# Kernel tuning notes

Hardware: AMD Instinct MI355X
Metric: run time of the kernel (lower is better)

The kernel has to match this reference:

```python
import jax, jax.numpy as jnp
import numpy as np

B, N, D_IN, D_MODEL = 8, 384, 512, 512


def gen_masking_matrix(n):
    # Vectorized port of the numba _gen_matrix: a[i, j, k] True iff k lies in the
    # 'geometric attention' reachability band between query i and key j.
    I = np.arange(n)[:, None, None]
    J = np.arange(n)[None, :, None]
    K = np.arange(n)[None, None, :]
    lt = (I < J) & (((K > I) & (K < J)) | ((K >= 2 * I - J + 1) & (K < I)))
    gt = (I > J) & (((K > J) & (K < I)) | ((K > I) & (K <= 2 * I - J)))
    return jnp.asarray(lt | gt)  # (n, n, n) bool


def setup_inputs() -> dict:
    key = jax.random.key(0)
    ks = jax.random.split(key, 8)
    s_in = 1.0 / np.sqrt(D_IN)
    return {
        "h": jax.random.normal(ks[0], (B, N, D_IN), jnp.float32),
        "mask": jnp.ones((B, N), jnp.float32),
        "Wq": jax.random.normal(ks[1], (D_MODEL, D_IN), jnp.float32) * s_in,
        "bq": jax.random.normal(ks[2], (D_MODEL,), jnp.float32) * 0.01,
        "Wk": jax.random.normal(ks[3], (D_MODEL, D_IN), jnp.float32) * s_in,
        "wlr": jax.random.normal(ks[4], (1, D_IN), jnp.float32) * s_in,
        "blr": jnp.zeros((1,), jnp.float32),
        "wrl": jax.random.normal(ks[5], (1, D_IN), jnp.float32) * s_in,
        "brl": jnp.zeros((1,), jnp.float32),
        "alpha": jnp.array([1.0 / np.sqrt(D_MODEL)], jnp.float32),
        "beta": jnp.array([1.0], jnp.float32),
        "gamma": jnp.array([0.0], jnp.float32),
        "masking_matrix": gen_masking_matrix(N),
    }


def reference(h, mask, Wq, bq, Wk, wlr, blr, wrl, brl, alpha, beta, gamma, masking_matrix):
    n = h.shape[1]
    dt = h.dtype
    q = h @ Wq.T + bq                       # (B, n, d_model)
    k = h @ Wk.T                            # (B, n, d_model)
    left = h @ wlr.T + blr                  # (B, n, 1)
    right = h @ wrl.T + brl                 # (B, n, 1)
    iu = jnp.triu(jnp.ones((n, n), dt))
    il = jnp.tril(jnp.ones((n, n), dt), -1)
    d = left * iu + right * il              # (B, n, n)
    scores = jnp.einsum("bnd,bmd->bnm", q, k)
    raw = jnp.clip(alpha * scores + beta * d + gamma, -16.0, 14.0)
    log_p = jax.nn.log_sigmoid(raw)         # log sigmoid(raw)
    log_1mp = jnp.log1p(-jnp.exp(log_p))    # log(1 - sigmoid(raw))
    # a[b,i,j] = sum_k mask[i,j,k] * log_1mp[b,i,k] + log_p[b,i,j]
    a = jnp.einsum("ijk,bik->bij", masking_matrix.astype(dt), log_1mp) + log_p
    r = a - 10000.0 * jnp.eye(n, dtype=dt)
    alignment_mask = mask[:, None, :] * mask[:, :, None]
    return r, alignment_mask
```

## Files before the change

kernel.cpp:

```cpp
#include <hip/hip_runtime.h>
#include <math.h>

#define N_SEQ 384
#define DIM 512
#define BATCH 8
#define M_ROWS (BATCH * N_SEQ)
#define QK_COLS (2 * DIM)

typedef short v8s __attribute__((ext_vector_type(8)));
typedef float v4f __attribute__((ext_vector_type(4)));

__device__ inline unsigned short f2bf(float f) {
    union { float f; unsigned u; } c; c.f = f;
    unsigned u = c.u;
    u += 0x7fffu + ((u >> 16) & 1u);
    return (unsigned short)(u >> 16);
}

__global__ __launch_bounds__(256) void prep(
    const float* __restrict__ h, const float* __restrict__ Wq,
    const float* __restrict__ Wk, const float* __restrict__ wlr,
    const float* __restrict__ blr, const float* __restrict__ wrl,
    const float* __restrict__ brl, unsigned short* __restrict__ h_bf,
    unsigned short* __restrict__ w_bf, float* __restrict__ left,
    float* __restrict__ right)
{
    const int wv = threadIdx.x >> 6, lane = threadIdx.x & 63;
    const int task = blockIdx.x * 4 + wv;
    const float* src; unsigned short* dst;
    if (task < M_ROWS) {
        src = h + (size_t)task * DIM;
        dst = h_bf + (size_t)task * DIM;
    } else {
        const int r = task - M_ROWS;
        src = (r < DIM) ? (Wq + (size_t)r * DIM) : (Wk + (size_t)(r - DIM) * DIM);
        dst = w_bf + (size_t)r * DIM;
    }
    const float4* s4 = (const float4*)src;
    const float4 v0 = s4[lane];
    const float4 v1 = s4[lane + 64];
    ushort4 o0, o1;
    o0.x = f2bf(v0.x); o0.y = f2bf(v0.y); o0.z = f2bf(v0.z); o0.w = f2bf(v0.w);
    o1.x = f2bf(v1.x); o1.y = f2bf(v1.y); o1.z = f2bf(v1.z); o1.w = f2bf(v1.w);
    *(ushort4*)(dst + lane * 4)       = o0;
    *(ushort4*)(dst + 256 + lane * 4) = o1;
    if (task < M_ROWS) {
        const float4* wl4 = (const float4*)wlr;
        const float4* wr4 = (const float4*)wrl;
        const float4 a0 = wl4[lane], a1 = wl4[lane + 64];
        const float4 c0 = wr4[lane], c1 = wr4[lane + 64];
        float sl = v0.x * a0.x + v0.y * a0.y + v0.z * a0.z + v0.w * a0.w
                 + v1.x * a1.x + v1.y * a1.y + v1.z * a1.z + v1.w * a1.w;
        float sr = v0.x * c0.x + v0.y * c0.y + v0.z * c0.z + v0.w * c0.w
                 + v1.x * c1.x + v1.y * c1.y + v1.z * c1.z + v1.w * c1.w;
#pragma unroll
        for (int off = 32; off > 0; off >>= 1) {
            sl += __shfl_down(sl, off);
            sr += __shfl_down(sr, off);
        }
        if (lane == 0) {
            left[task]  = sl + blr[0];
            right[task] = sr + brl[0];
        }
    }
}

__global__ __launch_bounds__(256) void qk_gemm(
    const unsigned short* __restrict__ A,
    const unsigned short* __restrict__ Bm,
    const float* __restrict__ bq,
    unsigned short* __restrict__ C)
{
    __shared__ unsigned short As[4][64][40];
    __shared__ unsigned short Bs[4][64][40];
    const int bm = blockIdx.x * 64;
    const int bn = blockIdx.y * 64;
    const int t = threadIdx.x;
    const int wv = t >> 6, lane = t & 63;
    const int wm = (wv & 1) * 32, wn = (wv >> 1) * 32;
    const int lm = lane & 15, quad = lane >> 4;
    const int srow = t >> 2, skc = (t & 3) * 8;
    v4f acc[2][2] = {};
    for (int k0 = 0; k0 < DIM; k0 += 128) {
        const unsigned short* ap = A  + (size_t)(bm + srow) * DIM + k0 + skc;
        const unsigned short* bp = Bm + (size_t)(bn + srow) * DIM + k0 + skc;
        v8s a[4], b[4];
#pragma unroll
        for (int q = 0; q < 4; ++q) {
            a[q] = *(const v8s*)(ap + q * 32);
            b[q] = *(const v8s*)(bp + q * 32);
        }
        __syncthreads();
#pragma unroll
        for (int q = 0; q < 4; ++q) {
            *(v8s*)&As[q][srow][skc] = a[q];
            *(v8s*)&Bs[q][srow][skc] = b[q];
        }
        __syncthreads();
#pragma unroll
        for (int half = 0; half < 4; ++half) {
            v8s af[2], bf[2];
#pragma unroll
            for (int i = 0; i < 2; ++i) af[i] = *(const v8s*)&As[half][wm + i * 16 + lm][quad * 8];
#pragma unroll
            for (int j = 0; j < 2; ++j) bf[j] = *(const v8s*)&Bs[half][wn + j * 16 + lm][quad * 8];
#pragma unroll
            for (int i = 0; i < 2; ++i)
#pragma unroll
                for (int j = 0; j < 2; ++j)
                    acc[i][j] = __builtin_amdgcn_mfma_f32_16x16x32_bf16(af[i], bf[j], acc[i][j], 0, 0, 0);
        }
    }
#pragma unroll
    for (int i = 0; i < 2; ++i)
#pragma unroll
        for (int j = 0; j < 2; ++j) {
            const int col = bn + wn + j * 16 + lm;
            const float bias = (col < DIM) ? bq[col] : 0.f;
#pragma unroll
            for (int r = 0; r < 4; ++r) {
                const int row = bm + wm + i * 16 + quad * 4 + r;
                C[(size_t)row * QK_COLS + col] = f2bf(acc[i][j][r] + bias);
            }
        }
}

__global__ __launch_bounds__(256) void score_gemm(
    const unsigned short* __restrict__ QK, const float* __restrict__ left,
    const float* __restrict__ right, const float* __restrict__ alpha,
    const float* __restrict__ beta, const float* __restrict__ gamma,
    float* __restrict__ raw)
{
    __shared__ unsigned short As[4][64][40];
    __shared__ unsigned short Bs[4][64][40];
    const int b  = blockIdx.z;
    const int bi = blockIdx.x * 64, bj = blockIdx.y * 64;
    const int t = threadIdx.x;
    const int wv = t >> 6, lane = t & 63;
    const int wm = (wv & 1) * 32, wn = (wv >> 1) * 32;
    const int lm = lane & 15, quad = lane >> 4;
    const int srow = t >> 2, skc = (t & 3) * 8;
    const unsigned short* qb = QK + (size_t)(b * N_SEQ) * QK_COLS;
    v4f acc[2][2] = {};
    for (int k0 = 0; k0 < DIM; k0 += 128) {
        const unsigned short* ap = qb + (size_t)(bi + srow) * QK_COLS + k0 + skc;
        const unsigned short* bp = qb + (size_t)(bj + srow) * QK_COLS + DIM + k0 + skc;
        v8s a[4], b4[4];
#pragma unroll
        for (int q = 0; q < 4; ++q) {
            a[q]  = *(const v8s*)(ap + q * 32);
            b4[q] = *(const v8s*)(bp + q * 32);
        }
        __syncthreads();
#pragma unroll
        for (int q = 0; q < 4; ++q) {
            *(v8s*)&As[q][srow][skc] = a[q];
            *(v8s*)&Bs[q][srow][skc] = b4[q];
        }
        __syncthreads();
#pragma unroll
        for (int half = 0; half < 4; ++half) {
            v8s af[2], bf[2];
#pragma unroll
            for (int i = 0; i < 2; ++i) af[i] = *(const v8s*)&As[half][wm + i * 16 + lm][quad * 8];
#pragma unroll
            for (int j = 0; j < 2; ++j) bf[j] = *(const v8s*)&Bs[half][wn + j * 16 + lm][quad * 8];
#pragma unroll
            for (int i = 0; i < 2; ++i)
#pragma unroll
                for (int j = 0; j < 2; ++j)
                    acc[i][j] = __builtin_amdgcn_mfma_f32_16x16x32_bf16(af[i], bf[j], acc[i][j], 0, 0, 0);
        }
    }
    const float al = alpha[0], be = beta[0], ga = gamma[0];
#pragma unroll
    for (int i = 0; i < 2; ++i)
#pragma unroll
        for (int j = 0; j < 2; ++j) {
            const int jcol = bj + wn + j * 16 + lm;
#pragma unroll
            for (int r = 0; r < 4; ++r) {
                const int irow = bi + wm + i * 16 + quad * 4 + r;
                const float lv = left[b * N_SEQ + irow];
                const float rv = right[b * N_SEQ + irow];
                const float dterm = (jcol >= irow) ? lv : rv;
                float v = fmaf(al, acc[i][j][r], fmaf(be, dterm, ga));
                v = fminf(fmaxf(v, -16.f), 14.f);
                raw[((size_t)b * N_SEQ + irow) * N_SEQ + jcol] = v;
            }
        }
}

__global__ __launch_bounds__(256) void finalize(
    const float* __restrict__ raw, const float* __restrict__ mask,
    float* __restrict__ out_r, float* __restrict__ out_am)
{
    const int n = N_SEQ;
    __shared__ float P[4][N_SEQ + 1];
    const int wv = threadIdx.x >> 6, lane = threadIdx.x & 63;
    const int b = blockIdx.y;
    const int i = blockIdx.x * 4 + wv;
    const float* rowp = raw + ((size_t)b * n + i) * n;

    float x[6], l1[6];
#pragma unroll
    for (int c = 0; c < 6; ++c) {
        x[c]  = rowp[c * 64 + lane];
        l1[c] = -log1pf(expf(x[c]));
    }
    float base = 0.f;
#pragma unroll
    for (int c = 0; c < 6; ++c) {
        float incl = l1[c];
#pragma unroll
        for (int off = 1; off < 64; off <<= 1) {
            const float tt = __shfl_up(incl, off);
            if (lane >= off) incl += tt;
        }
        P[wv][1 + c * 64 + lane] = base + incl;
        base += __shfl(incl, 63);
    }
    if (lane == 0) P[wv][0] = 0.f;
    __syncthreads();

    const float mi = mask[b * n + i];
#pragma unroll
    for (int c = 0; c < 6; ++c) {
        const int j = c * 64 + lane;
        float s = 0.f;
        if (i < j) {
            int lo2 = 2 * i - j + 1; if (lo2 < 0) lo2 = 0;
            s = (P[wv][j] - P[wv][i + 1]) + (P[wv][i] - P[wv][lo2]);
        } else if (i > j) {
            int hi2 = 2 * i - j + 1; if (hi2 > n) hi2 = n;
            s = (P[wv][i] - P[wv][j + 1]) + (P[wv][hi2] - P[wv][i + 1]);
        }
        float r = s + (x[c] + l1[c]);
        if (i == j) r -= 10000.f;
        const size_t o = ((size_t)b * n + i) * n + j;
        out_r[o]  = r;
        out_am[o] = mi * mask[b * n + j];
    }
}

extern "C" void kernel_launch(void* const* d_in, const int* in_sizes, int n_in,
                              void* d_out, int out_size, void* d_ws, size_t ws_size,
                              hipStream_t stream) {
    const float* h     = (const float*)d_in[0];
    const float* mask  = (const float*)d_in[1];
    const float* Wq    = (const float*)d_in[2];
    const float* bq    = (const float*)d_in[3];
    const float* Wk    = (const float*)d_in[4];
    const float* wlr   = (const float*)d_in[5];
    const float* blr   = (const float*)d_in[6];
    const float* wrl   = (const float*)d_in[7];
    const float* brl   = (const float*)d_in[8];
    const float* alpha = (const float*)d_in[9];
    const float* beta  = (const float*)d_in[10];
    const float* gamma = (const float*)d_in[11];

    unsigned short* h_bf  = (unsigned short*)d_ws;
    unsigned short* w_bf  = h_bf + (size_t)M_ROWS * DIM;
    unsigned short* qk_bf = w_bf + (size_t)QK_COLS * DIM;
    float* left  = (float*)(qk_bf + (size_t)M_ROWS * QK_COLS);
    float* right = left + M_ROWS;
    float* raw   = right + M_ROWS;

    float* out_r  = (float*)d_out;
    float* out_am = out_r + (size_t)BATCH * N_SEQ * N_SEQ;

    prep<<<1024, 256, 0, stream>>>(h, Wq, Wk, wlr, blr, wrl, brl,
                                   h_bf, w_bf, left, right);
    dim3 g1(M_ROWS / 64, QK_COLS / 64);
    qk_gemm<<<g1, 256, 0, stream>>>(h_bf, w_bf, bq, qk_bf);
    dim3 g2(N_SEQ / 64, N_SEQ / 64, BATCH);
    score_gemm<<<g2, 256, 0, stream>>>(qk_bf, left, right, alpha, beta, gamma, raw);
    dim3 g3(M_ROWS / 4 / BATCH, BATCH);
    finalize<<<g3, 256, 0, stream>>>(raw, mask, out_r, out_am);
}
```

Baseline: 301.9 us.

## Fuse score GEMM with scan finalize, keeping raw scores in LDS

Merges score_gemm and finalize into one kernel where each block computes 16 full query rows (all 384 keys) via MFMA. Q rows are staged in XOR-swizzled LDS and K is streamed straight from global memory with register double-buffering. The clipped scores stay in shared memory for the prefix-sum finalize, so the raw intermediate no longer goes through global memory and one launch is removed. In exchange the grid shrinks to 192 blocks, and each K tile is re-read from global/L2 by every block with no LDS reuse, which may lower occupancy and parallelism.

```diff
diff --git a/kernel.cpp b/kernel.cpp
--- a/kernel.cpp
+++ b/kernel.cpp
@@ -125,121 +125,122 @@
         }
 }
 
-__global__ __launch_bounds__(256) void score_gemm(
+__global__ __launch_bounds__(256) void score_final(
     const unsigned short* __restrict__ QK, const float* __restrict__ left,
     const float* __restrict__ right, const float* __restrict__ alpha,
     const float* __restrict__ beta, const float* __restrict__ gamma,
-    float* __restrict__ raw)
+    const float* __restrict__ mask, float* __restrict__ out_r,
+    float* __restrict__ out_am)
 {
-    __shared__ unsigned short As[4][64][40];
-    __shared__ unsigned short Bs[4][64][40];
-    const int b  = blockIdx.z;
-    const int bi = blockIdx.x * 64, bj = blockIdx.y * 64;
+    __shared__ unsigned short q_lds[16 * 512];
+    __shared__ float sp[16][N_SEQ + 1];
+    const int b  = blockIdx.y;
+    const int i0 = blockIdx.x * 16;
     const int t = threadIdx.x;
     const int wv = t >> 6, lane = t & 63;
-    const int wm = (wv & 1) * 32, wn = (wv >> 1) * 32;
     const int lm = lane & 15, quad = lane >> 4;
-    const int srow = t >> 2, skc = (t & 3) * 8;
-    const unsigned short* qb = QK + (size_t)(b * N_SEQ) * QK_COLS;
-    v4f acc[2][2] = {};
-    for (int k0 = 0; k0 < DIM; k0 += 128) {
-        const unsigned short* ap = qb + (size_t)(bi + srow) * QK_COLS + k0 + skc;
-        const unsigned short* bp = qb + (size_t)(bj + srow) * QK_COLS + DIM + k0 + skc;
-        v8s a[4], b4[4];
-#pragma unroll
-        for (int q = 0; q < 4; ++q) {
-            a[q]  = *(const v8s*)(ap + q * 32);
-            b4[q] = *(const v8s*)(bp + q * 32);
-        }
-        __syncthreads();
-#pragma unroll
-        for (int q = 0; q < 4; ++q) {
-            *(v8s*)&As[q][srow][skc] = a[q];
-            *(v8s*)&Bs[q][srow][skc] = b4[q];
-        }
-        __syncthreads();
-#pragma unroll
-        for (int half = 0; half < 4; ++half) {
-            v8s af[2], bf[2];
-#pragma unroll
-            for (int i = 0; i < 2; ++i) af[i] = *(const v8s*)&As[half][wm + i * 16 + lm][quad * 8];
-#pragma unroll
-            for (int j = 0; j < 2; ++j) bf[j] = *(const v8s*)&Bs[half][wn + j * 16 + lm][quad * 8];
-#pragma unroll
-            for (int i = 0; i < 2; ++i)
-#pragma unroll
-                for (int j = 0; j < 2; ++j)
-                    acc[i][j] = __builtin_amdgcn_mfma_f32_16x16x32_bf16(af[i], bf[j], acc[i][j], 0, 0, 0);
-        }
-    }
+    const int wn = wv * 96;
+
+#pragma unroll
+    for (int it = 0; it < 4; ++it) {
+        const int ch  = t + 256 * it;
+        const int row = ch >> 6, c = ch & 63;
+        const v8s v = *(const v8s*)(QK + (size_t)(b * N_SEQ + i0 + row) * QK_COLS + c * 8);
+        *(v8s*)&q_lds[row * 512 + ((c ^ (row & 7)) << 3)] = v;
+    }
+    __syncthreads();
+
+    const unsigned short* kb = QK + (size_t)(b * N_SEQ) * QK_COLS + DIM;
+    const unsigned short* kr[6];
+#pragma unroll
+    for (int j = 0; j < 6; ++j)
+        kr[j] = kb + (size_t)(wn + j * 16 + lm) * QK_COLS + quad * 8;
+
+    v4f acc[6] = {};
+    v8s bc[6];
+#pragma unroll
+    for (int j = 0; j < 6; ++j) bc[j] = *(const v8s*)(kr[j]);
+#pragma unroll
+    for (int ks = 0; ks < 16; ++ks) {
+        v8s bn[6];
+        if (ks < 15) {
+#pragma unroll
+            for (int j = 0; j < 6; ++j) bn[j] = *(const v8s*)(kr[j] + (ks + 1) * 32);
+        }
+        const v8s af = *(const v8s*)&q_lds[lm * 512 + ((((ks << 2) + quad) ^ (lm & 7)) << 3)];
+#pragma unroll
+        for (int j = 0; j < 6; ++j)
+            acc[j] = __builtin_amdgcn_mfma_f32_16x16x32_bf16(af, bc[j], acc[j], 0, 0, 0);
+        if (ks < 15) {
+#pragma unroll
+            for (int j = 0; j < 6; ++j) bc[j] = bn[j];
+        }
+    }
+
     const float al = alpha[0], be = beta[0], ga = gamma[0];
-#pragma unroll
-    for (int i = 0; i < 2; ++i)
-#pragma unroll
-        for (int j = 0; j < 2; ++j) {
-            const int jcol = bj + wn + j * 16 + lm;
-#pragma unroll
-            for (int r = 0; r < 4; ++r) {
-                const int irow = bi + wm + i * 16 + quad * 4 + r;
-                const float lv = left[b * N_SEQ + irow];
-                const float rv = right[b * N_SEQ + irow];
-                const float dterm = (jcol >= irow) ? lv : rv;
-                float v = fmaf(al, acc[i][j][r], fmaf(be, dterm, ga));
-                v = fminf(fmaxf(v, -16.f), 14.f);
-                raw[((size_t)b * N_SEQ + irow) * N_SEQ + jcol] = v;
+    float lvr[4], rvr[4];
+#pragma unroll
+    for (int r = 0; r < 4; ++r) {
+        lvr[r] = left [b * N_SEQ + i0 + quad * 4 + r];
+        rvr[r] = right[b * N_SEQ + i0 + quad * 4 + r];
+    }
+#pragma unroll
+    for (int j = 0; j < 6; ++j) {
+        const int jcol = wn + j * 16 + lm;
+#pragma unroll
+        for (int r = 0; r < 4; ++r) {
+            const int gi = i0 + quad * 4 + r;
+            const float dterm = (jcol >= gi) ? lvr[r] : rvr[r];
+            float v = fmaf(al, acc[j][r], fmaf(be, dterm, ga));
+            v = fminf(fmaxf(v, -16.f), 14.f);
+            sp[quad * 4 + r][jcol] = v;
+        }
+    }
+    __syncthreads();
+
+    for (int rr = 0; rr < 4; ++rr) {
+        const int irow = wv * 4 + rr;
+        const int gi = i0 + irow;
+        float x[6], l1[6];
+#pragma unroll
+        for (int c = 0; c < 6; ++c) {
+            x[c]  = sp[irow][c * 64 + lane];
+            l1[c] = -log1pf(expf(x[c]));
+        }
+        float base = 0.f;
+#pragma unroll
+        for (int c = 0; c < 6; ++c) {
+            float incl = l1[c];
+#pragma unroll
+            for (int off = 1; off < 64; off <<= 1) {
+                const float tt = __shfl_up(incl, off);
+                if (lane >= off) incl += tt;
             }
-        }
-}
-
-__global__ __launch_bounds__(256) void finalize(
-    const float* __restrict__ raw, const float* __restrict__ mask,
-    float* __restrict__ out_r, float* __restrict__ out_am)
-{
-    const int n = N_SEQ;
-    __shared__ float P[4][N_SEQ + 1];
-    const int wv = threadIdx.x >> 6, lane = threadIdx.x & 63;
-    const int b = blockIdx.y;
-    const int i = blockIdx.x * 4 + wv;
-    const float* rowp = raw + ((size_t)b * n + i) * n;
-
-    float x[6], l1[6];
-#pragma unroll
-    for (int c = 0; c < 6; ++c) {
-        x[c]  = rowp[c * 64 + lane];
-        l1[c] = -log1pf(expf(x[c]));
-    }
-    float base = 0.f;
-#pragma unroll
-    for (int c = 0; c < 6; ++c) {
-        float incl = l1[c];
-#pragma unroll
-        for (int off = 1; off < 64; off <<= 1) {
-            const float tt = __shfl_up(incl, off);
-            if (lane >= off) incl += tt;
-        }
-        P[wv][1 + c * 64 + lane] = base + incl;
-        base += __shfl(incl, 63);
-    }
-    if (lane == 0) P[wv][0] = 0.f;
-    __syncthreads();
-
-    const float mi = mask[b * n + i];
-#pragma unroll
-    for (int c = 0; c < 6; ++c) {
-        const int j = c * 64 + lane;
-        float s = 0.f;
-        if (i < j) {
-            int lo2 = 2 * i - j + 1; if (lo2 < 0) lo2 = 0;
-            s = (P[wv][j] - P[wv][i + 1]) + (P[wv][i] - P[wv][lo2]);
-        } else if (i > j) {
-            int hi2 = 2 * i - j + 1; if (hi2 > n) hi2 = n;
-            s = (P[wv][i] - P[wv][j + 1]) + (P[wv][hi2] - P[wv][i + 1]);
-        }
-        float r = s + (x[c] + l1[c]);
-        if (i == j) r -= 10000.f;
-        const size_t o = ((size_t)b * n + i) * n + j;
-        out_r[o]  = r;
-        out_am[o] = mi * mask[b * n + j];
+            sp[irow][1 + c * 64 + lane] = base + incl;
+            base += __shfl(incl, 63);
+        }
+        if (lane == 0) sp[irow][0] = 0.f;
+        asm volatile("" ::: "memory");
+
+        const float mi = mask[b * N_SEQ + gi];
+        const float* P = sp[irow];
+#pragma unroll
+        for (int c = 0; c < 6; ++c) {
+            const int j = c * 64 + lane;
+            float s = 0.f;
+            if (gi < j) {
+                int lo2 = 2 * gi - j + 1; if (lo2 < 0) lo2 = 0;
+                s = (P[j] - P[gi + 1]) + (P[gi] - P[lo2]);
+            } else if (gi > j) {
+                int hi2 = 2 * gi - j + 1; if (hi2 > N_SEQ) hi2 = N_SEQ;
+                s = (P[gi] - P[j + 1]) + (P[hi2] - P[gi + 1]);
+            }
+            float r = s + (x[c] + l1[c]);
+            if (gi == j) r -= 10000.f;
+            const size_t o = ((size_t)b * N_SEQ + gi) * N_SEQ + j;
+            out_r[o]  = r;
+            out_am[o] = mi * mask[b * N_SEQ + j];
+        }
     }
 }
 
@@ -264,7 +265,6 @@
     unsigned short* qk_bf = w_bf + (size_t)QK_COLS * DIM;
     float* left  = (float*)(qk_bf + (size_t)M_ROWS * QK_COLS);
     float* right = left + M_ROWS;
-    float* raw   = right + M_ROWS;
 
     float* out_r  = (float*)d_out;
     float* out_am = out_r + (size_t)BATCH * N_SEQ * N_SEQ;
@@ -273,8 +273,7 @@
                                    h_bf, w_bf, left, right);
     dim3 g1(M_ROWS / 64, QK_COLS / 64);
     qk_gemm<<<g1, 256, 0, stream>>>(h_bf, w_bf, bq, qk_bf);
-    dim3 g2(N_SEQ / 64, N_SEQ / 64, BATCH);
-    score_gemm<<<g2, 256, 0, stream>>>(qk_bf, left, right, alpha, beta, gamma, raw);
-    dim3 g3(M_ROWS / 4 / BATCH, BATCH);
-    finalize<<<g3, 256, 0, stream>>>(raw, mask, out_r, out_am);
-}
+    dim3 g2(N_SEQ / 16, BATCH);
+    score_final<<<g2, 256, 0, stream>>>(qk_bf, left, right, alpha, beta, gamma,
+                                        mask, out_r, out_am);
+}
```

New measurement: 316.3 us. +4.8%, slower.

## Stage GEMM tiles via direct global-to-LDS loads with XOR-swizzled layout

Applied to the files above, without the earlier changes.

Both the QK projection GEMM and the score GEMM now fill shared memory with global_load_lds (16-byte direct-to-LDS loads) instead of loading into registers and then storing to LDS. The padded [4][64][40] tile layout is replaced by an unpadded 64x128 tile whose 16-byte chunks are XOR-swizzled by row, so MFMA fragment reads avoid bank conflicts. This removes the register round trip and VGPR pressure from staging. It depends on the 16-byte direct-LDS load being supported on this target, and the loads are still not double-buffered.

```diff
diff --git a/kernel.cpp b/kernel.cpp
--- a/kernel.cpp
+++ b/kernel.cpp
@@ -71,39 +71,49 @@
     const float* __restrict__ bq,
     unsigned short* __restrict__ C)
 {
-    __shared__ unsigned short As[4][64][40];
-    __shared__ unsigned short Bs[4][64][40];
+    __shared__ unsigned short As[64 * 128];
+    __shared__ unsigned short Bs[64 * 128];
     const int bm = blockIdx.x * 64;
     const int bn = blockIdx.y * 64;
     const int t = threadIdx.x;
     const int wv = t >> 6, lane = t & 63;
     const int wm = (wv & 1) * 32, wn = (wv >> 1) * 32;
     const int lm = lane & 15, quad = lane >> 4;
-    const int srow = t >> 2, skc = (t & 3) * 8;
+    const int sbase = wv * 16;
+    const int rsub  = lane >> 4;
+    const int cdst  = lane & 15;
     v4f acc[2][2] = {};
     for (int k0 = 0; k0 < DIM; k0 += 128) {
-        const unsigned short* ap = A  + (size_t)(bm + srow) * DIM + k0 + skc;
-        const unsigned short* bp = Bm + (size_t)(bn + srow) * DIM + k0 + skc;
-        v8s a[4], b[4];
-#pragma unroll
-        for (int q = 0; q < 4; ++q) {
-            a[q] = *(const v8s*)(ap + q * 32);
-            b[q] = *(const v8s*)(bp + q * 32);
-        }
         __syncthreads();
 #pragma unroll
-        for (int q = 0; q < 4; ++q) {
-            *(v8s*)&As[q][srow][skc] = a[q];
-            *(v8s*)&Bs[q][srow][skc] = b[q];
+        for (int i = 0; i < 4; ++i) {
+            const int row  = sbase + i * 4 + rsub;
+            const int clog = cdst ^ (row & 7);
+            const unsigned short* ga = A  + (size_t)(bm + row) * DIM + k0 + clog * 8;
+            const unsigned short* gb = Bm + (size_t)(bn + row) * DIM + k0 + clog * 8;
+            __builtin_amdgcn_global_load_lds(
+                (const __attribute__((address_space(1))) unsigned*)ga,
+                (__attribute__((address_space(3))) unsigned*)&As[(sbase + i * 4) * 128],
+                16, 0, 0);
+            __builtin_amdgcn_global_load_lds(
+                (const __attribute__((address_space(1))) unsigned*)gb,
+                (__attribute__((address_space(3))) unsigned*)&Bs[(sbase + i * 4) * 128],
+                16, 0, 0);
         }
         __syncthreads();
 #pragma unroll
-        for (int half = 0; half < 4; ++half) {
+        for (int h = 0; h < 4; ++h) {
             v8s af[2], bf[2];
 #pragma unroll
-            for (int i = 0; i < 2; ++i) af[i] = *(const v8s*)&As[half][wm + i * 16 + lm][quad * 8];
-#pragma unroll
-            for (int j = 0; j < 2; ++j) bf[j] = *(const v8s*)&Bs[half][wn + j * 16 + lm][quad * 8];
+            for (int i = 0; i < 2; ++i) {
+                const int r = wm + i * 16 + lm;
+                af[i] = *(const v8s*)&As[r * 128 + (((h * 4 + quad) ^ (r & 7)) << 3)];
+            }
+#pragma unroll
+            for (int j = 0; j < 2; ++j) {
+                const int r = wn + j * 16 + lm;
+                bf[j] = *(const v8s*)&Bs[r * 128 + (((h * 4 + quad) ^ (r & 7)) << 3)];
+            }
 #pragma unroll
             for (int i = 0; i < 2; ++i)
 #pragma unroll
@@ -131,40 +141,50 @@
     const float* __restrict__ beta, const float* __restrict__ gamma,
     float* __restrict__ raw)
 {
-    __shared__ unsigned short As[4][64][40];
-    __shared__ unsigned short Bs[4][64][40];
+    __shared__ unsigned short As[64 * 128];
+    __shared__ unsigned short Bs[64 * 128];
     const int b  = blockIdx.z;
     const int bi = blockIdx.x * 64, bj = blockIdx.y * 64;
     const int t = threadIdx.x;
     const int wv = t >> 6, lane = t & 63;
     const int wm = (wv & 1) * 32, wn = (wv >> 1) * 32;
     const int lm = lane & 15, quad = lane >> 4;
-    const int srow = t >> 2, skc = (t & 3) * 8;
+    const int sbase = wv * 16;
+    const int rsub  = lane >> 4;
+    const int cdst  = lane & 15;
     const unsigned short* qb = QK + (size_t)(b * N_SEQ) * QK_COLS;
     v4f acc[2][2] = {};
     for (int k0 = 0; k0 < DIM; k0 += 128) {
-        const unsigned short* ap = qb + (size_t)(bi + srow) * QK_COLS + k0 + skc;
-        const unsigned short* bp = qb + (size_t)(bj + srow) * QK_COLS + DIM + k0 + skc;
-        v8s a[4], b4[4];
-#pragma unroll
-        for (int q = 0; q < 4; ++q) {
-            a[q]  = *(const v8s*)(ap + q * 32);
-            b4[q] = *(const v8s*)(bp + q * 32);
-        }
         __syncthreads();
 #pragma unroll
-        for (int q = 0; q < 4; ++q) {
-            *(v8s*)&As[q][srow][skc] = a[q];
-            *(v8s*)&Bs[q][srow][skc] = b4[q];
+        for (int i = 0; i < 4; ++i) {
+            const int row  = sbase + i * 4 + rsub;
+            const int clog = cdst ^ (row & 7);
+            const unsigned short* ga = qb + (size_t)(bi + row) * QK_COLS + k0 + clog * 8;
+            const unsigned short* gb = qb + (size_t)(bj + row) * QK_COLS + DIM + k0 + clog * 8;
+            __builtin_amdgcn_global_load_lds(
+                (const __attribute__((address_space(1))) unsigned*)ga,
+                (__attribute__((address_space(3))) unsigned*)&As[(sbase + i * 4) * 128],
+                16, 0, 0);
+            __builtin_amdgcn_global_load_lds(
+                (const __attribute__((address_space(1))) unsigned*)gb,
+                (__attribute__((address_space(3))) unsigned*)&Bs[(sbase + i * 4) * 128],
+                16, 0, 0);
         }
         __syncthreads();
 #pragma unroll
-        for (int half = 0; half < 4; ++half) {
+        for (int h = 0; h < 4; ++h) {
             v8s af[2], bf[2];
 #pragma unroll
-            for (int i = 0; i < 2; ++i) af[i] = *(const v8s*)&As[half][wm + i * 16 + lm][quad * 8];
-#pragma unroll
-            for (int j = 0; j < 2; ++j) bf[j] = *(const v8s*)&Bs[half][wn + j * 16 + lm][quad * 8];
+            for (int i = 0; i < 2; ++i) {
+                const int r = wm + i * 16 + lm;
+                af[i] = *(const v8s*)&As[r * 128 + (((h * 4 + quad) ^ (r & 7)) << 3)];
+            }
+#pragma unroll
+            for (int j = 0; j < 2; ++j) {
+                const int r = wn + j * 16 + lm;
+                bf[j] = *(const v8s*)&Bs[r * 128 + (((h * 4 + quad) ^ (r & 7)) << 3)];
+            }
 #pragma unroll
             for (int i = 0; i < 2; ++i)
 #pragma unroll
```

New measurement: 302.7 us. About the same (+0.3%).
